# Optimization experiments

Measured on AMD Instinct MI355X. Metric: run time of the kernel, lower is better.

Reference implementation:

```python
import jax, jax.numpy as jnp
import numpy as np

B, S, D, H = 4, 2048, 2048, 16
DK = D // H  # 128
EPS = 1e-6


def setup_inputs() -> dict:
    key = jax.random.key(0)
    ks = jax.random.split(key, 8)
    scale = 1.0 / np.sqrt(D)
    return {
        "q": jax.random.normal(ks[0], (B, S, D), jnp.float32),
        "k": jax.random.normal(ks[1], (B, S, D), jnp.float32),
        "v": jax.random.normal(ks[2], (B, S, D), jnp.float32),
        "Wq": jax.random.normal(ks[3], (D, D), jnp.float32) * scale,
        "Wk": jax.random.normal(ks[4], (D, D), jnp.float32) * scale,
        "Wv": jax.random.normal(ks[5], (D, D), jnp.float32) * scale,
        "Wo": jax.random.normal(ks[6], (D, D), jnp.float32) * scale,
        "gamma": jnp.ones((D,), jnp.float32),
        "beta": jnp.zeros((D,), jnp.float32),
    }


def reference(q, k, v, Wq, Wk, Wv, Wo, gamma, beta):
    residual = q
    # projections (Linear with weight (out,in): x @ W^T)
    Q = (q @ Wq.T).reshape(B, S, H, DK)
    K = (k @ Wk.T).reshape(B, S, H, DK)
    V = (v @ Wv.T).reshape(B, S, H, DK)
    # faithful to source: permute(2,0,1,3) then flatten -> head-major (H*B, S, DK)
    Q = jnp.transpose(Q, (2, 0, 1, 3)).reshape(H * B, S, DK)
    K = jnp.transpose(K, (2, 0, 1, 3)).reshape(H * B, S, DK)
    V = jnp.transpose(V, (2, 0, 1, 3)).reshape(H * B, S, DK)
    scores = jnp.einsum("nqd,nkd->nqk", Q, K) / jnp.sqrt(jnp.float32(DK))
    attn = jax.nn.softmax(scores, axis=-1)  # (H*B, S, S)
    context = jnp.einsum("nqk,nkd->nqd", attn, V)
    # faithful to source: view (H*B,S,DK) as (B,H,S,DK) (batch-major reinterpretation)
    context = context.reshape(B, H, S, DK)
    context = jnp.transpose(context, (0, 2, 1, 3)).reshape(B, S, H * DK)
    output = context @ Wo.T  # dropout=0.0 (eval)
    output = output + residual
    mean = jnp.mean(output, axis=-1, keepdims=True)
    var = jnp.mean(jnp.square(output - mean), axis=-1, keepdims=True)
    output = (output - mean) / jnp.sqrt(var + EPS) * gamma + beta
    return output, attn
```

## Files before the change

### kernel.cpp

```cpp
#include <hip/hip_runtime.h>
#include <cstdint>

typedef __attribute__((ext_vector_type(8))) short short8;
typedef __attribute__((ext_vector_type(4))) float f32x4;
typedef __attribute__((ext_vector_type(2))) unsigned u32x2;
typedef unsigned short ushort_t;

constexpr int Bc = 4, Sc = 2048, Dc = 2048, Hc = 16, DKc = 128;
constexpr long NTOK = (long)Bc * Sc;
constexpr long OUT_ELEMS = NTOK * (long)Dc;
constexpr float SCALE = 0.08838834764831843f;

__device__ __forceinline__ ushort_t f2bf(float f) {
  unsigned u = __builtin_bit_cast(unsigned, f);
  u = (u + 0x7FFFu + ((u >> 16) & 1u)) >> 16;
  return (ushort_t)u;
}

__device__ __forceinline__ short8 pack8(const f32x4& a, const f32x4& b) {
  short8 h;
  h[0] = (short)f2bf(a[0]); h[1] = (short)f2bf(a[1]);
  h[2] = (short)f2bf(a[2]); h[3] = (short)f2bf(a[3]);
  h[4] = (short)f2bf(b[0]); h[5] = (short)f2bf(b[1]);
  h[6] = (short)f2bf(b[2]); h[7] = (short)f2bf(b[3]);
  return h;
}

__device__ __forceinline__ void gl2lds16(const ushort_t* g, ushort_t* l) {
  __builtin_amdgcn_global_load_lds(
      (__attribute__((address_space(1))) unsigned int*)(g),
      (__attribute__((address_space(3))) unsigned int*)(l), 16, 0, 0);
}

__device__ __forceinline__ void bar() {
  asm volatile("" ::: "memory");
  __builtin_amdgcn_s_barrier();
  asm volatile("" ::: "memory");
}

__global__ __launch_bounds__(512, 2)
void proj_gemm(const float* __restrict__ qf, const float* __restrict__ kf,
               const float* __restrict__ vf,
               const ushort_t* __restrict__ Wqb, const ushort_t* __restrict__ Wkb,
               const ushort_t* __restrict__ Wvb,
               ushort_t* __restrict__ Qb, ushort_t* __restrict__ Kb,
               ushort_t* __restrict__ VTo)
{
  __shared__ __align__(16) ushort_t SM[2][2][2][128 * 64];

  const int z = blockIdx.z;
  const float* Afull = (z == 0) ? qf : (z == 1) ? kf : vf;
  const ushort_t* Bp = (z == 0) ? Wqb : (z == 1) ? Wkb : Wvb;
  ushort_t* Cp = (z == 0) ? Qb : (z == 1) ? Kb : VTo;

  const int tid = threadIdx.x, lane = tid & 63, wave = tid >> 6;
  const int wm = wave >> 2, wn = wave & 3;

  const int lin = blockIdx.y * 8 + blockIdx.x;
  const int swz = (lin & 7) * 32 + (lin >> 3);
  const long n0 = (long)(swz & 7) * 256;
  const long m0 = (long)(swz >> 3) * 256;

  constexpr int NT = 32;

  const float*    Ag = Afull + m0 * (long)Dc;
  const ushort_t* Bg = Bp + n0 * (long)Dc;

  auto stageB = [&](ushort_t* dst, int kt, int ht) {
#pragma unroll
    for (int c = 0; c < 2; ++c) {
      int U = (c * 8 + wave) * 64 + lane;
      int row = U >> 3, p = U & 7, u = p ^ (row & 7);
      gl2lds16(Bg + (long)(ht * 128 + row) * Dc + kt * 64 + u * 8,
               dst + (c * 8 + wave) * 512);
    }
  };
  auto loadA = [&](int kt, f32x4 alo[2][2], f32x4 ahi[2][2]) {
#pragma unroll
    for (int ht = 0; ht < 2; ++ht)
#pragma unroll
      for (int c = 0; c < 2; ++c) {
        int U = (c * 8 + wave) * 64 + lane;
        int row = U >> 3, p = U & 7, u = p ^ (row & 7);
        const float* g = Ag + (long)(ht * 128 + row) * Dc + kt * 64 + u * 8;
        alo[ht][c] = *(const f32x4*)g;
        ahi[ht][c] = *(const f32x4*)(g + 4);
      }
  };
  auto writeA = [&](int buf, const f32x4 alo[2][2], const f32x4 ahi[2][2]) {
#pragma unroll
    for (int ht = 0; ht < 2; ++ht)
#pragma unroll
      for (int c = 0; c < 2; ++c) {
        int chunk = c * 8 + wave;
        *(short8*)(&SM[0][buf][ht][chunk * 512 + lane * 8]) =
            pack8(alo[ht][c], ahi[ht][c]);
      }
  };

  stageB(&SM[1][0][0][0], 0, 0);
  stageB(&SM[1][0][1][0], 0, 1);
  stageB(&SM[1][1][0][0], 1, 0);
  {
    f32x4 alo[2][2], ahi[2][2];
    loadA(0, alo, ahi);
    asm volatile("s_waitcnt vmcnt(0)" ::: "memory");
    writeA(0, alo, ahi);
    asm volatile("s_waitcnt lgkmcnt(0)" ::: "memory");
  }
  __builtin_amdgcn_s_barrier();
  asm volatile("" ::: "memory");

  f32x4 acc[8][4] = {};

  for (int kt = 0; kt < NT; ++kt) {
    const int cur = kt & 1;
    const ushort_t* Acur = &SM[0][cur][0][0];
    const ushort_t* Bcur = &SM[1][cur][0][0];
    const int k1 = (kt + 1) & (NT - 1);
    const int k2 = (kt + 2) & (NT - 1);
    short8 af[4][2], bq0[2][2], bq1[2][2];
    f32x4 alo[2][2], ahi[2][2];

#pragma unroll
    for (int mf = 0; mf < 4; ++mf)
#pragma unroll
      for (int ks = 0; ks < 2; ++ks) {
        int r = mf * 16 + (lane & 15);
        int u = ks * 4 + (lane >> 4), p = u ^ (r & 7);
        af[mf][ks] = *(const short8*)(Acur + wm * (128 * 64) + r * 64 + p * 8);
      }
#pragma unroll
    for (int nf = 0; nf < 2; ++nf)
#pragma unroll
      for (int ks = 0; ks < 2; ++ks) {
        int r = (wn & 1) * 64 + nf * 16 + (lane & 15);
        int u = ks * 4 + (lane >> 4), p = u ^ (r & 7);
        bq0[nf][ks] = *(const short8*)(Bcur + (wn >> 1) * (128 * 64) + r * 64 + p * 8);
      }
    stageB(&SM[1][cur ^ 1][1][0], k1, 1);
    bar();
    __builtin_amdgcn_s_setprio(1);
#pragma unroll
    for (int mf = 0; mf < 4; ++mf)
#pragma unroll
      for (int nf = 0; nf < 2; ++nf)
#pragma unroll
        for (int ks = 0; ks < 2; ++ks)
          acc[mf][nf] = __builtin_amdgcn_mfma_f32_16x16x32_bf16(af[mf][ks], bq0[nf][ks], acc[mf][nf], 0, 0, 0);
    __builtin_amdgcn_s_setprio(0);
    bar();

#pragma unroll
    for (int nf = 0; nf < 2; ++nf)
#pragma unroll
      for (int ks = 0; ks < 2; ++ks) {
        int r = (wn & 1) * 64 + 32 + nf * 16 + (lane & 15);
        int u = ks * 4 + (lane >> 4), p = u ^ (r & 7);
        bq1[nf][ks] = *(const short8*)(Bcur + (wn >> 1) * (128 * 64) + r * 64 + p * 8);
      }
    loadA(k1, alo, ahi);
    bar();
    __builtin_amdgcn_s_setprio(1);
#pragma unroll
    for (int mf = 0; mf < 4; ++mf)
#pragma unroll
      for (int nf = 0; nf < 2; ++nf)
#pragma unroll
        for (int ks = 0; ks < 2; ++ks)
          acc[mf][2 + nf] = __builtin_amdgcn_mfma_f32_16x16x32_bf16(af[mf][ks], bq1[nf][ks], acc[mf][2 + nf], 0, 0, 0);
    __builtin_amdgcn_s_setprio(0);
    bar();

#pragma unroll
    for (int mf = 0; mf < 4; ++mf)
#pragma unroll
      for (int ks = 0; ks < 2; ++ks) {
        int r = 64 + mf * 16 + (lane & 15);
        int u = ks * 4 + (lane >> 4), p = u ^ (r & 7);
        af[mf][ks] = *(const short8*)(Acur + wm * (128 * 64) + r * 64 + p * 8);
      }
    stageB(&SM[1][cur][0][0], k2, 0);
    bar();
    __builtin_amdgcn_s_setprio(1);
#pragma unroll
    for (int mf = 0; mf < 4; ++mf)
#pragma unroll
      for (int nf = 0; nf < 2; ++nf)
#pragma unroll
        for (int ks = 0; ks < 2; ++ks)
          acc[4 + mf][nf] = __builtin_amdgcn_mfma_f32_16x16x32_bf16(af[mf][ks], bq0[nf][ks], acc[4 + mf][nf], 0, 0, 0);
    __builtin_amdgcn_s_setprio(0);
    bar();

    asm volatile("s_waitcnt vmcnt(2)" ::: "memory");
    writeA(cur ^ 1, alo, ahi);
    asm volatile("s_waitcnt lgkmcnt(0)" ::: "memory");
    bar();
    __builtin_amdgcn_s_setprio(1);
#pragma unroll
    for (int mf = 0; mf < 4; ++mf)
#pragma unroll
      for (int nf = 0; nf < 2; ++nf)
#pragma unroll
        for (int ks = 0; ks < 2; ++ks)
          acc[4 + mf][2 + nf] = __builtin_amdgcn_mfma_f32_16x16x32_bf16(af[mf][ks], bq1[nf][ks], acc[4 + mf][2 + nf], 0, 0, 0);
    __builtin_amdgcn_s_setprio(0);
    bar();
  }

  asm volatile("s_waitcnt vmcnt(0)" ::: "memory");

  if (z == 2) {
    bar();
    char* Tb = (char*)&SM[0][0][0][0];
#pragma unroll
    for (int mq = 0; mq < 8; ++mq) {
#pragma unroll
      for (int nq = 0; nq < 4; ++nq) {
        int rg = wm * 128 + (mq >> 2) * 64 + (mq & 3) * 16 + ((lane >> 4) * 4);
        int cg = wn * 64 + (nq >> 1) * 32 + (nq & 1) * 16 + (lane & 15);
        u32x2 t;
        t[0] = (unsigned)f2bf(acc[mq][nq][0]) | ((unsigned)f2bf(acc[mq][nq][1]) << 16);
        t[1] = (unsigned)f2bf(acc[mq][nq][2]) | ((unsigned)f2bf(acc[mq][nq][3]) << 16);
        int off = cg * 512 + (((rg >> 3) ^ (cg & 31)) * 16) + (rg & 7) * 2;
        *(u32x2*)(Tb + off) = t;
      }
    }
    bar();
    const long bq = m0 >> 11;
    const long s0 = m0 & 2047;
#pragma unroll
    for (int i = 0; i < 16; ++i) {
      int row = i * 16 + (tid >> 5);
      int un  = tid & 31;
      int p = un ^ (row & 31);
      short8 val = *(const short8*)(Tb + row * 512 + p * 16);
      long cgg = n0 + row;
      long vtrow = ((cgg >> 7) * 4 + bq) * 128 + (cgg & 127);
      *(short8*)(&Cp[vtrow * (long)Sc + s0 + un * 8]) = val;
    }
  } else {
#pragma unroll
    for (int mq = 0; mq < 8; ++mq) {
#pragma unroll
      for (int nq = 0; nq < 4; ++nq) {
#pragma unroll
        for (int j = 0; j < 4; ++j) {
          long rg = m0 + wm * 128 + (mq >> 2) * 64 + (mq & 3) * 16 + ((lane >> 4) * 4) + j;
          long cg = n0 + wn * 64 + (nq >> 1) * 32 + (nq & 1) * 16 + (lane & 15);
          Cp[rg * (long)Dc + cg] = f2bf(acc[mq][nq][j]);
        }
      }
    }
  }
}

__global__ __launch_bounds__(512, 2)
void out_gemm(const ushort_t* __restrict__ Ap, const ushort_t* __restrict__ Bp,
              float* __restrict__ Cp, const float* __restrict__ residual)
{
  __shared__ __align__(16) ushort_t SM[2][2][2][128 * 64];

  const int tid = threadIdx.x, lane = tid & 63, wave = tid >> 6;
  const int wm = wave >> 2, wn = wave & 3;
  const int lin = blockIdx.y * 8 + blockIdx.x;
  const int swz = (lin & 7) * 32 + (lin >> 3);
  const long n0 = (long)(swz & 7) * 256;
  const long m0 = (long)(swz >> 3) * 256;
  constexpr int NT = 32;

  const ushort_t* Ag = Ap + m0 * (long)Dc;
  const ushort_t* Bg = Bp + n0 * (long)Dc;

  auto stage = [&](const ushort_t* gb, ushort_t* dst, int kt, int ht) {
#pragma unroll
    for (int c = 0; c < 2; ++c) {
      int U = (c * 8 + wave) * 64 + lane;
      int row = U >> 3, p = U & 7, u = p ^ (row & 7);
      gl2lds16(gb + (long)(ht * 128 + row) * Dc + kt * 64 + u * 8,
               dst + (c * 8 + wave) * 512);
    }
  };

  stage(Bg, &SM[1][0][0][0], 0, 0);
  stage(Ag, &SM[0][0][0][0], 0, 0);
  stage(Bg, &SM[1][0][1][0], 0, 1);
  stage(Ag, &SM[0][0][1][0], 0, 1);
  stage(Bg, &SM[1][1][0][0], 1, 0);
  stage(Ag, &SM[0][1][0][0], 1, 0);
  asm volatile("s_waitcnt vmcnt(4)" ::: "memory");
  __builtin_amdgcn_s_barrier();
  asm volatile("" ::: "memory");

  f32x4 acc[8][4] = {};

  for (int kt = 0; kt < NT; ++kt) {
    const int cur = kt & 1;
    const ushort_t* Acur = &SM[0][cur][0][0];
    const ushort_t* Bcur = &SM[1][cur][0][0];
    const int k1 = (kt + 1) & (NT - 1);
    const int k2 = (kt + 2) & (NT - 1);
    short8 af[4][2], bq0[2][2], bq1[2][2];

#pragma unroll
    for (int mf = 0; mf < 4; ++mf)
#pragma unroll
      for (int ks = 0; ks < 2; ++ks) {
        int r = mf * 16 + (lane & 15);
        int u = ks * 4 + (lane >> 4), p = u ^ (r & 7);
        af[mf][ks] = *(const short8*)(Acur + wm * (128 * 64) + r * 64 + p * 8);
      }
#pragma unroll
    for (int nf = 0; nf < 2; ++nf)
#pragma unroll
      for (int ks = 0; ks < 2; ++ks) {
        int r = (wn & 1) * 64 + nf * 16 + (lane & 15);
        int u = ks * 4 + (lane >> 4), p = u ^ (r & 7);
        bq0[nf][ks] = *(const short8*)(Bcur + (wn >> 1) * (128 * 64) + r * 64 + p * 8);
      }
    stage(Bg, &SM[1][cur ^ 1][1][0], k1, 1);
    bar();
    __builtin_amdgcn_s_setprio(1);
#pragma unroll
    for (int mf = 0; mf < 4; ++mf)
#pragma unroll
      for (int nf = 0; nf < 2; ++nf)
#pragma unroll
        for (int ks = 0; ks < 2; ++ks)
          acc[mf][nf] = __builtin_amdgcn_mfma_f32_16x16x32_bf16(af[mf][ks], bq0[nf][ks], acc[mf][nf], 0, 0, 0);
    __builtin_amdgcn_s_setprio(0);
    bar();

#pragma unroll
    for (int nf = 0; nf < 2; ++nf)
#pragma unroll
      for (int ks = 0; ks < 2; ++ks) {
        int r = (wn & 1) * 64 + 32 + nf * 16 + (lane & 15);
        int u = ks * 4 + (lane >> 4), p = u ^ (r & 7);
        bq1[nf][ks] = *(const short8*)(Bcur + (wn >> 1) * (128 * 64) + r * 64 + p * 8);
      }
    stage(Ag, &SM[0][cur ^ 1][1][0], k1, 1);
    bar();
    __builtin_amdgcn_s_setprio(1);
#pragma unroll
    for (int mf = 0; mf < 4; ++mf)
#pragma unroll
      for (int nf = 0; nf < 2; ++nf)
#pragma unroll
        for (int ks = 0; ks < 2; ++ks)
          acc[mf][2 + nf] = __builtin_amdgcn_mfma_f32_16x16x32_bf16(af[mf][ks], bq1[nf][ks], acc[mf][2 + nf], 0, 0, 0);
    __builtin_amdgcn_s_setprio(0);
    bar();

#pragma unroll
    for (int mf = 0; mf < 4; ++mf)
#pragma unroll
      for (int ks = 0; ks < 2; ++ks) {
        int r = 64 + mf * 16 + (lane & 15);
        int u = ks * 4 + (lane >> 4), p = u ^ (r & 7);
        af[mf][ks] = *(const short8*)(Acur + wm * (128 * 64) + r * 64 + p * 8);
      }
    stage(Bg, &SM[1][cur][0][0], k2, 0);
    bar();
    __builtin_amdgcn_s_setprio(1);
#pragma unroll
    for (int mf = 0; mf < 4; ++mf)
#pragma unroll
      for (int nf = 0; nf < 2; ++nf)
#pragma unroll
        for (int ks = 0; ks < 2; ++ks)
          acc[4 + mf][nf] = __builtin_amdgcn_mfma_f32_16x16x32_bf16(af[mf][ks], bq0[nf][ks], acc[4 + mf][nf], 0, 0, 0);
    __builtin_amdgcn_s_setprio(0);
    bar();

    stage(Ag, &SM[0][cur][0][0], k2, 0);
    asm volatile("s_waitcnt vmcnt(4)" ::: "memory");
    bar();
    __builtin_amdgcn_s_setprio(1);
#pragma unroll
    for (int mf = 0; mf < 4; ++mf)
#pragma unroll
      for (int nf = 0; nf < 2; ++nf)
#pragma unroll
        for (int ks = 0; ks < 2; ++ks)
          acc[4 + mf][2 + nf] = __builtin_amdgcn_mfma_f32_16x16x32_bf16(af[mf][ks], bq1[nf][ks], acc[4 + mf][2 + nf], 0, 0, 0);
    __builtin_amdgcn_s_setprio(0);
    bar();
  }

  asm volatile("s_waitcnt vmcnt(0)" ::: "memory");

#pragma unroll
  for (int mq = 0; mq < 8; ++mq) {
#pragma unroll
    for (int nq = 0; nq < 4; ++nq) {
#pragma unroll
      for (int j = 0; j < 4; ++j) {
        long rg = m0 + wm * 128 + (mq >> 2) * 64 + (mq & 3) * 16 + ((lane >> 4) * 4) + j;
        long cg = n0 + wn * 64 + (nq >> 1) * 32 + (nq & 1) * 16 + (lane & 15);
        Cp[rg * (long)Dc + cg] = acc[mq][nq][j] + residual[rg * (long)Dc + cg];
      }
    }
  }
}

__global__ __launch_bounds__(256, 2)
void flash_attn(const ushort_t* __restrict__ Qb, const ushort_t* __restrict__ Kb,
                const ushort_t* __restrict__ VT, float* __restrict__ attn,
                ushort_t* __restrict__ Cb)
{
  __shared__ __align__(16) ushort_t Qs[128 * 128];
  __shared__ __align__(16) ushort_t Ks[64 * 128];
  __shared__ __align__(16) ushort_t Vs[128 * 64];
  __shared__ __align__(16) ushort_t Ps[128 * 64];

  const int tid = threadIdx.x, lane = tid & 63, wave = tid >> 6;
  const int wr = wave >> 1, wc = wave & 1;

  const int bid = blockIdx.x;
  const int xcd = bid & 7, slot = bid >> 3;
  const int n = xcd * 8 + (slot >> 4);
  const long m0 = (long)(slot & 15) * 128;
  const int b = n & 3, h = n >> 2;

  const ushort_t* Qg = Qb + ((long)b * Sc) * Dc + (long)h * DKc;
  const ushort_t* Kg = Kb + ((long)b * Sc) * Dc + (long)h * DKc;
  const ushort_t* Vg = VT + (long)n * DKc * (long)Sc;
  float* Pg = attn + (long)n * Sc * (long)Sc;

#pragma unroll
  for (int c8 = 0; c8 < 8; ++c8) {
    int chunk = c8 * 4 + wave;
    int U = chunk * 64 + lane;
    int row = U >> 4, p = U & 15, u = p ^ (row & 15);
    gl2lds16(Qg + (m0 + row) * (long)Dc + u * 8, &Qs[chunk * 512]);
  }

  auto kaddr = [&](int t, int c4) -> const short8* {
    int chunk = c4 * 4 + wave;
    int U = chunk * 64 + lane;
    int row = U >> 4, p = U & 15, u = p ^ (row & 15);
    return (const short8*)(Kg + ((long)t * 64 + row) * (long)Dc + u * 8);
  };
  auto vaddr = [&](int t, int c4) -> const short8* {
    int chunk = c4 * 4 + wave;
    int U = chunk * 64 + lane;
    int row = U >> 3, p = U & 7, u = p ^ (row & 7);
    return (const short8*)(Vg + (long)row * Sc + (long)t * 64 + u * 8);
  };

  float rs[4][4] = {};

  short8 kr0 = *kaddr(0, 0), kr1 = *kaddr(0, 1), kr2_ = *kaddr(0, 2), kr3 = *kaddr(0, 3);
  for (int t = 0; t < 32; ++t) {
    __syncthreads();
    *(short8*)(&Ks[(0 * 4 + wave) * 512 + lane * 8]) = kr0;
    *(short8*)(&Ks[(1 * 4 + wave) * 512 + lane * 8]) = kr1;
    *(short8*)(&Ks[(2 * 4 + wave) * 512 + lane * 8]) = kr2_;
    *(short8*)(&Ks[(3 * 4 + wave) * 512 + lane * 8]) = kr3;
    {
      int tn = (t + 1) & 31;
      kr0 = *kaddr(tn, 0); kr1 = *kaddr(tn, 1);
      kr2_ = *kaddr(tn, 2); kr3 = *kaddr(tn, 3);
    }
    __syncthreads();
    f32x4 acc[4][2] = {};
#pragma unroll
    for (int kk = 0; kk < 4; ++kk) {
      short8 af[4], bfr[2];
#pragma unroll
      for (int m = 0; m < 4; ++m) {
        int row = wr * 64 + m * 16 + (lane & 15);
        int p = (kk * 4 + (lane >> 4)) ^ (row & 15);
        af[m] = *(const short8*)(&Qs[row * 128 + p * 8]);
      }
#pragma unroll
      for (int nn = 0; nn < 2; ++nn) {
        int row = wc * 32 + nn * 16 + (lane & 15);
        int p = (kk * 4 + (lane >> 4)) ^ (row & 15);
        bfr[nn] = *(const short8*)(&Ks[row * 128 + p * 8]);
      }
#pragma unroll
      for (int m = 0; m < 4; ++m)
#pragma unroll
        for (int nn = 0; nn < 2; ++nn)
          acc[m][nn] = __builtin_amdgcn_mfma_f32_16x16x32_bf16(af[m], bfr[nn], acc[m][nn], 0, 0, 0);
    }
#pragma unroll
    for (int m = 0; m < 4; ++m)
#pragma unroll
      for (int nn = 0; nn < 2; ++nn)
#pragma unroll
        for (int j = 0; j < 4; ++j)
          rs[m][j] += __expf(acc[m][nn][j] * SCALE);
  }

  short8 k0 = *kaddr(0, 0), k1_ = *kaddr(0, 1), k2_ = *kaddr(0, 2), k3 = *kaddr(0, 3);
  short8 v0 = *vaddr(0, 0), v1 = *vaddr(0, 1), v2 = *vaddr(0, 2), v3 = *vaddr(0, 3);

  float* red = (float*)Ps;
#pragma unroll
  for (int m = 0; m < 4; ++m)
#pragma unroll
    for (int j = 0; j < 4; ++j) {
#pragma unroll
      for (int off = 1; off < 16; off <<= 1)
        rs[m][j] += __shfl_xor(rs[m][j], off);
    }
  __syncthreads();
  if ((lane & 15) == 0) {
#pragma unroll
    for (int m = 0; m < 4; ++m)
#pragma unroll
      for (int j = 0; j < 4; ++j)
        red[wc * 128 + wr * 64 + m * 16 + ((lane >> 4) * 4) + j] = rs[m][j];
  }
  __syncthreads();
  float invl[4][4];
#pragma unroll
  for (int m = 0; m < 4; ++m)
#pragma unroll
    for (int j = 0; j < 4; ++j) {
      int row = wr * 64 + m * 16 + ((lane >> 4) * 4) + j;
      invl[m][j] = 1.f / (red[row] + red[128 + row]);
    }

  f32x4 acco[4][4] = {};
  for (int t = 0; t < 32; ++t) {
    __syncthreads();
    *(short8*)(&Ks[(0 * 4 + wave) * 512 + lane * 8]) = k0;
    *(short8*)(&Ks[(1 * 4 + wave) * 512 + lane * 8]) = k1_;
    *(short8*)(&Ks[(2 * 4 + wave) * 512 + lane * 8]) = k2_;
    *(short8*)(&Ks[(3 * 4 + wave) * 512 + lane * 8]) = k3;
    *(short8*)(&Vs[(0 * 4 + wave) * 512 + lane * 8]) = v0;
    *(short8*)(&Vs[(1 * 4 + wave) * 512 + lane * 8]) = v1;
    *(short8*)(&Vs[(2 * 4 + wave) * 512 + lane * 8]) = v2;
    *(short8*)(&Vs[(3 * 4 + wave) * 512 + lane * 8]) = v3;
    {
      int tn = (t + 1) & 31;
      k0 = *kaddr(tn, 0); k1_ = *kaddr(tn, 1); k2_ = *kaddr(tn, 2); k3 = *kaddr(tn, 3);
      v0 = *vaddr(tn, 0); v1 = *vaddr(tn, 1); v2 = *vaddr(tn, 2); v3 = *vaddr(tn, 3);
    }
    __syncthreads();
    f32x4 acc[4][2] = {};
#pragma unroll
    for (int kk = 0; kk < 4; ++kk) {
      short8 af[4], bfr[2];
#pragma unroll
      for (int m = 0; m < 4; ++m) {
        int row = wr * 64 + m * 16 + (lane & 15);
        int p = (kk * 4 + (lane >> 4)) ^ (row & 15);
        af[m] = *(const short8*)(&Qs[row * 128 + p * 8]);
      }
#pragma unroll
      for (int nn = 0; nn < 2; ++nn) {
        int row = wc * 32 + nn * 16 + (lane & 15);
        int p = (kk * 4 + (lane >> 4)) ^ (row & 15);
        bfr[nn] = *(const short8*)(&Ks[row * 128 + p * 8]);
      }
#pragma unroll
      for (int m = 0; m < 4; ++m)
#pragma unroll
        for (int nn = 0; nn < 2; ++nn)
          acc[m][nn] = __builtin_amdgcn_mfma_f32_16x16x32_bf16(af[m], bfr[nn], acc[m][nn], 0, 0, 0);
    }
#pragma unroll
    for (int m = 0; m < 4; ++m) {
#pragma unroll
      for (int nn = 0; nn < 2; ++nn) {
#pragma unroll
        for (int j = 0; j < 4; ++j) {
          float e = __expf(acc[m][nn][j] * SCALE) * invl[m][j];
          int row = wr * 64 + m * 16 + ((lane >> 4) * 4) + j;
          int col = wc * 32 + nn * 16 + (lane & 15);
          __builtin_nontemporal_store(e, &Pg[(m0 + row) * (long)Sc + (long)t * 64 + col]);
          int pp = (col >> 3) ^ (row & 7);
          Ps[row * 64 + pp * 8 + (col & 7)] = (ushort_t)f2bf(e);
        }
      }
    }
    __syncthreads();
#pragma unroll
    for (int ks = 0; ks < 2; ++ks) {
      short8 pa[4], vb[4];
#pragma unroll
      for (int m = 0; m < 4; ++m) {
        int row = wr * 64 + m * 16 + (lane & 15);
        int p = (ks * 4 + (lane >> 4)) ^ (row & 7);
        pa[m] = *(const short8*)(&Ps[row * 64 + p * 8]);
      }
#pragma unroll
      for (int nn = 0; nn < 4; ++nn) {
        int row = wc * 64 + nn * 16 + (lane & 15);
        int p = (ks * 4 + (lane >> 4)) ^ (row & 7);
        vb[nn] = *(const short8*)(&Vs[row * 64 + p * 8]);
      }
#pragma unroll
      for (int m = 0; m < 4; ++m)
#pragma unroll
        for (int nn = 0; nn < 4; ++nn)
          acco[m][nn] = __builtin_amdgcn_mfma_f32_16x16x32_bf16(pa[m], vb[nn], acco[m][nn], 0, 0, 0);
    }
  }

#pragma unroll
  for (int m = 0; m < 4; ++m) {
#pragma unroll
    for (int nn = 0; nn < 4; ++nn) {
#pragma unroll
      for (int j = 0; j < 4; ++j) {
        int row = wr * 64 + m * 16 + ((lane >> 4) * 4) + j;
        int col = wc * 64 + nn * 16 + (lane & 15);
        Cb[((long)(n >> 4) * Sc + m0 + row) * (long)Dc + (long)(n & 15) * DKc + col] =
            (ushort_t)f2bf(acco[m][nn][j]);
      }
    }
  }
}

__global__ __launch_bounds__(256)
void castW_bf16(const float* __restrict__ w0, const float* __restrict__ w1,
                const float* __restrict__ w2, const float* __restrict__ w3,
                ushort_t* __restrict__ o0, ushort_t* __restrict__ o1,
                ushort_t* __restrict__ o2, ushort_t* __restrict__ o3) {
  const float* in; ushort_t* out;
  switch (blockIdx.y) {
    case 0: in = w0; out = o0; break;
    case 1: in = w1; out = o1; break;
    case 2: in = w2; out = o2; break;
    default: in = w3; out = o3; break;
  }
  long i = ((long)blockIdx.x * 256 + threadIdx.x) * 8;
  f32x4 x = *(const f32x4*)(in + i);
  f32x4 y = *(const f32x4*)(in + i + 4);
  *(short8*)(out + i) = pack8(x, y);
}

__global__ __launch_bounds__(256)
void layernorm_rows(float* __restrict__ out, const float* __restrict__ gamma,
                    const float* __restrict__ beta) {
  const long row = blockIdx.x;
  float* p = out + row * (long)Dc;
  const int tid = threadIdx.x;
  const int lane = tid & 63, wave = tid >> 6;
  f32x4 v0 = *(const f32x4*)(p + tid * 8);
  f32x4 v1 = *(const f32x4*)(p + tid * 8 + 4);
  float s = 0.f, ss = 0.f;
#pragma unroll
  for (int e = 0; e < 4; ++e) { s += v0[e]; ss += v0[e] * v0[e]; }
#pragma unroll
  for (int e = 0; e < 4; ++e) { s += v1[e]; ss += v1[e] * v1[e]; }
  for (int off = 32; off > 0; off >>= 1) { s += __shfl_xor(s, off); ss += __shfl_xor(ss, off); }
  __shared__ float rs_[4], rss_[4];
  if (lane == 0) { rs_[wave] = s; rss_[wave] = ss; }
  __syncthreads();
  s  = rs_[0] + rs_[1] + rs_[2] + rs_[3];
  ss = rss_[0] + rss_[1] + rss_[2] + rss_[3];
  const float mean = s * (1.f / Dc);
  const float var  = ss * (1.f / Dc) - mean * mean;
  const float rstd = rsqrtf(var + 1e-6f);
  f32x4 g0 = *(const f32x4*)(gamma + tid * 8);
  f32x4 g1 = *(const f32x4*)(gamma + tid * 8 + 4);
  f32x4 b0 = *(const f32x4*)(beta + tid * 8);
  f32x4 b1 = *(const f32x4*)(beta + tid * 8 + 4);
#pragma unroll
  for (int e = 0; e < 4; ++e) v0[e] = (v0[e] - mean) * rstd * g0[e] + b0[e];
#pragma unroll
  for (int e = 0; e < 4; ++e) v1[e] = (v1[e] - mean) * rstd * g1[e] + b1[e];
  *(f32x4*)(p + tid * 8) = v0;
  *(f32x4*)(p + tid * 8 + 4) = v1;
}

extern "C" void kernel_launch(void* const* d_in, const int* in_sizes, int n_in,
                              void* d_out, int out_size, void* d_ws, size_t ws_size,
                              hipStream_t stream) {
  (void)in_sizes; (void)n_in; (void)out_size; (void)ws_size;
  const float* q  = (const float*)d_in[0];
  const float* k  = (const float*)d_in[1];
  const float* v  = (const float*)d_in[2];
  const float* Wq = (const float*)d_in[3];
  const float* Wk = (const float*)d_in[4];
  const float* Wv = (const float*)d_in[5];
  const float* Wo = (const float*)d_in[6];
  const float* gamma = (const float*)d_in[7];
  const float* beta  = (const float*)d_in[8];

  float* out  = (float*)d_out;
  float* attn = out + OUT_ELEMS;

  ushort_t* Wqb = (ushort_t*)d_ws;
  ushort_t* Wkb = Wqb + (long)Dc * Dc;
  ushort_t* Wvb = Wkb + (long)Dc * Dc;
  ushort_t* Wob = Wvb + (long)Dc * Dc;
  ushort_t* Qb  = Wob + (long)Dc * Dc;
  ushort_t* Kb  = Qb + OUT_ELEMS;
  ushort_t* VT  = Kb + OUT_ELEMS;
  ushort_t* Cb  = VT + OUT_ELEMS;

  castW_bf16<<<dim3((long)Dc * Dc / 2048, 4), dim3(256), 0, stream>>>(
      Wq, Wk, Wv, Wo, Wqb, Wkb, Wvb, Wob);

  proj_gemm<<<dim3(8, 32, 3), dim3(512), 0, stream>>>(
      q, k, v, Wqb, Wkb, Wvb, Qb, Kb, VT);

  flash_attn<<<dim3(1024), dim3(256), 0, stream>>>(Qb, Kb, VT, attn, Cb);

  out_gemm<<<dim3(8, 32), dim3(512), 0, stream>>>(Cb, Wob, out, q);

  layernorm_rows<<<NTOK, dim3(256), 0, stream>>>(out, gamma, beta);
}
```

Measured before the change: 719.4 us.

## Double-buffer K/V via direct global-to-LDS loads and keep Q fragments in registers

Replaces register-staged K/V prefetch (global load into VGPRs, then store to LDS) with asynchronous direct global-to-LDS copies into ping-pong buffers, so each tile's load overlaps the previous tile's compute. Q MFMA fragments are loaded from LDS once into registers and reused across all key tiles, which frees the Q LDS region so the K/V buffers can alias it. Barriers become explicit waitcnt-plus-barrier sequences. This costs extra VGPRs for the held Q fragments, and it depends on hand-tuned vmcnt counts that assume a fixed number of in-flight nontemporal stores.

```diff
diff --git a/kernel.cpp b/kernel.cpp
--- a/kernel.cpp
+++ b/kernel.cpp
@@ -410,10 +410,9 @@
                 const ushort_t* __restrict__ VT, float* __restrict__ attn,
                 ushort_t* __restrict__ Cb)
 {
-  __shared__ __align__(16) ushort_t Qs[128 * 128];
-  __shared__ __align__(16) ushort_t Ks[64 * 128];
-  __shared__ __align__(16) ushort_t Vs[128 * 64];
-  __shared__ __align__(16) ushort_t Ps[128 * 64];
+  __shared__ __align__(16) ushort_t LDS[40960];
+  ushort_t* Qs = LDS;
+  ushort_t* Ps = LDS + 32768;
 
   const int tid = threadIdx.x, lane = tid & 63, wave = tid >> 6;
   const int wr = wave >> 1, wc = wave & 1;
@@ -429,6 +428,28 @@
   const ushort_t* Vg = VT + (long)n * DKc * (long)Sc;
   float* Pg = attn + (long)n * Sc * (long)Sc;
 
+  auto KsB = [&](int bf) -> ushort_t* { return LDS + (bf ? 0 : 16384); };
+  auto VsB = [&](int bf) -> ushort_t* { return LDS + (bf ? 8192 : 24576); };
+
+  auto stageK = [&](int t, ushort_t* dst) {
+#pragma unroll
+    for (int c4 = 0; c4 < 4; ++c4) {
+      int chunk = c4 * 4 + wave;
+      int U = chunk * 64 + lane;
+      int row = U >> 4, p = U & 15, u = p ^ (row & 15);
+      gl2lds16(Kg + ((long)t * 64 + row) * (long)Dc + u * 8, dst + chunk * 512);
+    }
+  };
+  auto stageV = [&](int t, ushort_t* dst) {
+#pragma unroll
+    for (int c4 = 0; c4 < 4; ++c4) {
+      int chunk = c4 * 4 + wave;
+      int U = chunk * 64 + lane;
+      int row = U >> 3, p = U & 7, u = p ^ (row & 7);
+      gl2lds16(Vg + (long)row * Sc + (long)t * 64 + u * 8, dst + chunk * 512);
+    }
+  };
+
 #pragma unroll
   for (int c8 = 0; c8 < 8; ++c8) {
     int chunk = c8 * 4 + wave;
@@ -436,56 +457,42 @@
     int row = U >> 4, p = U & 15, u = p ^ (row & 15);
     gl2lds16(Qg + (m0 + row) * (long)Dc + u * 8, &Qs[chunk * 512]);
   }
-
-  auto kaddr = [&](int t, int c4) -> const short8* {
-    int chunk = c4 * 4 + wave;
-    int U = chunk * 64 + lane;
-    int row = U >> 4, p = U & 15, u = p ^ (row & 15);
-    return (const short8*)(Kg + ((long)t * 64 + row) * (long)Dc + u * 8);
-  };
-  auto vaddr = [&](int t, int c4) -> const short8* {
-    int chunk = c4 * 4 + wave;
-    int U = chunk * 64 + lane;
-    int row = U >> 3, p = U & 7, u = p ^ (row & 7);
-    return (const short8*)(Vg + (long)row * Sc + (long)t * 64 + u * 8);
-  };
+  asm volatile("s_waitcnt vmcnt(0)" ::: "memory");
+  bar();
+  stageK(0, KsB(0));
+  short8 qf[4][4];
+#pragma unroll
+  for (int m = 0; m < 4; ++m)
+#pragma unroll
+    for (int kk = 0; kk < 4; ++kk) {
+      int row = wr * 64 + m * 16 + (lane & 15);
+      int p = (kk * 4 + (lane >> 4)) ^ (row & 15);
+      qf[m][kk] = *(const short8*)(&Qs[row * 128 + p * 8]);
+    }
+  asm volatile("s_waitcnt vmcnt(0) lgkmcnt(0)" ::: "memory");
+  bar();
 
   float rs[4][4] = {};
 
-  short8 kr0 = *kaddr(0, 0), kr1 = *kaddr(0, 1), kr2_ = *kaddr(0, 2), kr3 = *kaddr(0, 3);
   for (int t = 0; t < 32; ++t) {
-    __syncthreads();
-    *(short8*)(&Ks[(0 * 4 + wave) * 512 + lane * 8]) = kr0;
-    *(short8*)(&Ks[(1 * 4 + wave) * 512 + lane * 8]) = kr1;
-    *(short8*)(&Ks[(2 * 4 + wave) * 512 + lane * 8]) = kr2_;
-    *(short8*)(&Ks[(3 * 4 + wave) * 512 + lane * 8]) = kr3;
-    {
-      int tn = (t + 1) & 31;
-      kr0 = *kaddr(tn, 0); kr1 = *kaddr(tn, 1);
-      kr2_ = *kaddr(tn, 2); kr3 = *kaddr(tn, 3);
-    }
-    __syncthreads();
+    const ushort_t* Kcur = KsB(t & 1);
+    if (t < 31) stageK(t + 1, KsB((t & 1) ^ 1));
+    asm volatile("" ::: "memory");
     f32x4 acc[4][2] = {};
 #pragma unroll
     for (int kk = 0; kk < 4; ++kk) {
-      short8 af[4], bfr[2];
-#pragma unroll
-      for (int m = 0; m < 4; ++m) {
-        int row = wr * 64 + m * 16 + (lane & 15);
-        int p = (kk * 4 + (lane >> 4)) ^ (row & 15);
-        af[m] = *(const short8*)(&Qs[row * 128 + p * 8]);
-      }
+      short8 bfr[2];
 #pragma unroll
       for (int nn = 0; nn < 2; ++nn) {
         int row = wc * 32 + nn * 16 + (lane & 15);
         int p = (kk * 4 + (lane >> 4)) ^ (row & 15);
-        bfr[nn] = *(const short8*)(&Ks[row * 128 + p * 8]);
+        bfr[nn] = *(const short8*)(&Kcur[row * 128 + p * 8]);
       }
 #pragma unroll
       for (int m = 0; m < 4; ++m)
 #pragma unroll
         for (int nn = 0; nn < 2; ++nn)
-          acc[m][nn] = __builtin_amdgcn_mfma_f32_16x16x32_bf16(af[m], bfr[nn], acc[m][nn], 0, 0, 0);
+          acc[m][nn] = __builtin_amdgcn_mfma_f32_16x16x32_bf16(qf[m][kk], bfr[nn], acc[m][nn], 0, 0, 0);
     }
 #pragma unroll
     for (int m = 0; m < 4; ++m)
@@ -494,10 +501,9 @@
 #pragma unroll
         for (int j = 0; j < 4; ++j)
           rs[m][j] += __expf(acc[m][nn][j] * SCALE);
-  }
-
-  short8 k0 = *kaddr(0, 0), k1_ = *kaddr(0, 1), k2_ = *kaddr(0, 2), k3 = *kaddr(0, 3);
-  short8 v0 = *vaddr(0, 0), v1 = *vaddr(0, 1), v2 = *vaddr(0, 2), v3 = *vaddr(0, 3);
+    asm volatile("s_waitcnt vmcnt(0) lgkmcnt(0)" ::: "memory");
+    bar();
+  }
 
   float* red = (float*)Ps;
 #pragma unroll
@@ -508,7 +514,6 @@
       for (int off = 1; off < 16; off <<= 1)
         rs[m][j] += __shfl_xor(rs[m][j], off);
     }
-  __syncthreads();
   if ((lane & 15) == 0) {
 #pragma unroll
     for (int m = 0; m < 4; ++m)
@@ -526,44 +531,32 @@
       invl[m][j] = 1.f / (red[row] + red[128 + row]);
     }
 
+  stageK(0, KsB(0));
+  stageV(0, VsB(0));
+  asm volatile("s_waitcnt vmcnt(0) lgkmcnt(0)" ::: "memory");
+  bar();
+
   f32x4 acco[4][4] = {};
   for (int t = 0; t < 32; ++t) {
-    __syncthreads();
-    *(short8*)(&Ks[(0 * 4 + wave) * 512 + lane * 8]) = k0;
-    *(short8*)(&Ks[(1 * 4 + wave) * 512 + lane * 8]) = k1_;
-    *(short8*)(&Ks[(2 * 4 + wave) * 512 + lane * 8]) = k2_;
-    *(short8*)(&Ks[(3 * 4 + wave) * 512 + lane * 8]) = k3;
-    *(short8*)(&Vs[(0 * 4 + wave) * 512 + lane * 8]) = v0;
-    *(short8*)(&Vs[(1 * 4 + wave) * 512 + lane * 8]) = v1;
-    *(short8*)(&Vs[(2 * 4 + wave) * 512 + lane * 8]) = v2;
-    *(short8*)(&Vs[(3 * 4 + wave) * 512 + lane * 8]) = v3;
-    {
-      int tn = (t + 1) & 31;
-      k0 = *kaddr(tn, 0); k1_ = *kaddr(tn, 1); k2_ = *kaddr(tn, 2); k3 = *kaddr(tn, 3);
-      v0 = *vaddr(tn, 0); v1 = *vaddr(tn, 1); v2 = *vaddr(tn, 2); v3 = *vaddr(tn, 3);
-    }
-    __syncthreads();
+    const ushort_t* Kcur = KsB(t & 1);
+    const ushort_t* Vcur = VsB(t & 1);
+    if (t < 31) { stageK(t + 1, KsB((t & 1) ^ 1)); stageV(t + 1, VsB((t & 1) ^ 1)); }
+    asm volatile("" ::: "memory");
     f32x4 acc[4][2] = {};
 #pragma unroll
     for (int kk = 0; kk < 4; ++kk) {
-      short8 af[4], bfr[2];
-#pragma unroll
-      for (int m = 0; m < 4; ++m) {
-        int row = wr * 64 + m * 16 + (lane & 15);
-        int p = (kk * 4 + (lane >> 4)) ^ (row & 15);
-        af[m] = *(const short8*)(&Qs[row * 128 + p * 8]);
-      }
+      short8 bfr[2];
 #pragma unroll
       for (int nn = 0; nn < 2; ++nn) {
         int row = wc * 32 + nn * 16 + (lane & 15);
         int p = (kk * 4 + (lane >> 4)) ^ (row & 15);
-        bfr[nn] = *(const short8*)(&Ks[row * 128 + p * 8]);
+        bfr[nn] = *(const short8*)(&Kcur[row * 128 + p * 8]);
       }
 #pragma unroll
       for (int m = 0; m < 4; ++m)
 #pragma unroll
         for (int nn = 0; nn < 2; ++nn)
-          acc[m][nn] = __builtin_amdgcn_mfma_f32_16x16x32_bf16(af[m], bfr[nn], acc[m][nn], 0, 0, 0);
+          acc[m][nn] = __builtin_amdgcn_mfma_f32_16x16x32_bf16(qf[m][kk], bfr[nn], acc[m][nn], 0, 0, 0);
     }
 #pragma unroll
     for (int m = 0; m < 4; ++m) {
@@ -580,7 +573,8 @@
         }
       }
     }
-    __syncthreads();
+    asm volatile("s_waitcnt lgkmcnt(0)" ::: "memory");
+    bar();
 #pragma unroll
     for (int ks = 0; ks < 2; ++ks) {
       short8 pa[4], vb[4];
@@ -594,7 +588,7 @@
       for (int nn = 0; nn < 4; ++nn) {
         int row = wc * 64 + nn * 16 + (lane & 15);
         int p = (ks * 4 + (lane >> 4)) ^ (row & 7);
-        vb[nn] = *(const short8*)(&Vs[row * 64 + p * 8]);
+        vb[nn] = *(const short8*)(&Vcur[row * 64 + p * 8]);
       }
 #pragma unroll
       for (int m = 0; m < 4; ++m)
@@ -602,6 +596,8 @@
         for (int nn = 0; nn < 4; ++nn)
           acco[m][nn] = __builtin_amdgcn_mfma_f32_16x16x32_bf16(pa[m], vb[nn], acco[m][nn], 0, 0, 0);
     }
+    asm volatile("s_waitcnt vmcnt(32) lgkmcnt(0)" ::: "memory");
+    bar();
   }
 
 #pragma unroll
```

After: 1.064 ms. +47.9%, slower.
